# Optimization experiments

Hardware: AMD Instinct MI355X
Metric: run time of the kernel (lower is better)

## Reference

```python
import jax, jax.numpy as jnp
import numpy as np

NEG_SLOPE = 0.2

def setup_inputs() -> dict:
    key = jax.random.key(0)
    ks = jax.random.split(key, 10)
    N, E, L, D, H = 100000, 3200000, 200000, 128, 128
    x = jax.random.normal(ks[0], (N, D), dtype=jnp.float32)
    edge_index = jax.random.randint(ks[1], (2, E), 0, N, dtype=jnp.int64)
    edge_label_index = jax.random.randint(ks[2], (2, L), 0, N, dtype=jnp.int64)
    s = 1.0 / np.sqrt(D)
    W1l = jax.random.uniform(ks[3], (D, H), minval=-s, maxval=s, dtype=jnp.float32)
    b1 = jax.random.uniform(ks[4], (H,), minval=-s, maxval=s, dtype=jnp.float32)
    W1r = jax.random.uniform(ks[5], (D, H), minval=-s, maxval=s, dtype=jnp.float32)
    s2 = 1.0 / np.sqrt(H)
    W2l = jax.random.uniform(ks[6], (H, H), minval=-s2, maxval=s2, dtype=jnp.float32)
    b2 = jax.random.uniform(ks[7], (H,), minval=-s2, maxval=s2, dtype=jnp.float32)
    W2r = jax.random.uniform(ks[8], (H, H), minval=-s2, maxval=s2, dtype=jnp.float32)
    return {"x": x, "edge_index": edge_index, "edge_label_index": edge_label_index,
            "W1l": W1l, "b1": b1, "W1r": W1r, "W2l": W2l, "b2": b2, "W2r": W2r}

def reference(x, edge_index, edge_label_index, W1l, b1, W1r, W2l, b2, W2r):
    N = x.shape[0]
    src, dst = edge_index[0], edge_index[1]
    # in-degree for mean aggregation (clamped to avoid div-by-zero, matching mean over empty = 0)
    deg = jax.ops.segment_sum(jnp.ones_like(dst, dtype=x.dtype), dst, num_segments=N)
    inv_deg = (1.0 / jnp.maximum(deg, 1.0))[:, None]

    def sage(h, Wl, b, Wr):
        # mean of source-node features over incoming edges at each target node
        agg = jax.ops.segment_sum(h[src], dst, num_segments=N) * inv_deg
        return agg @ Wl + b + h @ Wr

    h = sage(x, W1l, b1, W1r)
    h = jnp.where(h >= 0, h, NEG_SLOPE * h)  # leaky_relu; eval mode so no dropout
    h = sage(h, W2l, b2, W2r)
    x_src = h[edge_label_index[0]]
    x_trg = h[edge_label_index[1]]
    return jnp.sum(x_src * x_trg, axis=1)
```

## Files before the change

kernel.cpp:

```cpp
#include <hip/hip_runtime.h>
#include <hip/hip_fp16.h>


#define D128 128
#define BSHIFT 9
#define BNODES 512

typedef __bf16 bf16x8 __attribute__((ext_vector_type(8)));
typedef float  f32x4  __attribute__((ext_vector_type(4)));
typedef _Float16 h2   __attribute__((ext_vector_type(2)));

union uh2cast { unsigned u; h2 h; };
__device__ inline h2 uash2(unsigned u) { uh2cast c; c.u = u; return c.h; }

__device__ inline unsigned short f2bf(float f) {
    unsigned u = __float_as_uint(f);
    u = u + 0x7FFF + ((u >> 16) & 1);
    return (unsigned short)(u >> 16);
}
__device__ inline float bf2f(unsigned short s) {
    return __uint_as_float(((unsigned)s) << 16);
}
__device__ inline unsigned packbf2(float lo, float hi) {
    return (unsigned)f2bf(lo) | ((unsigned)f2bf(hi) << 16);
}
__device__ inline unsigned char f2e5(float f) {
    unsigned short h = __half_as_ushort(__float2half(f));
    h = (unsigned short)(h + 0x7F + ((h >> 8) & 1));
    return (unsigned char)(h >> 8);
}


__global__ void cast_kernel(const float* __restrict__ in, unsigned short* __restrict__ outb,
                            unsigned char* __restrict__ out8, int n4) {
    int i = blockIdx.x * blockDim.x + threadIdx.x;
    if (i >= n4) return;
    float4 v = ((const float4*)in)[i];
    ushort4 ob;
    ob.x = f2bf(v.x); ob.y = f2bf(v.y); ob.z = f2bf(v.z); ob.w = f2bf(v.w);
    ((ushort4*)outb)[i] = ob;
    unsigned p = (unsigned)f2e5(v.x) | ((unsigned)f2e5(v.y) << 8) |
                 ((unsigned)f2e5(v.z) << 16) | ((unsigned)f2e5(v.w) << 24);
    ((unsigned*)out8)[i] = p;
}


__global__ void repack_kernel(const float* __restrict__ W1l, const float* __restrict__ W1r,
                              const float* __restrict__ W2l, const float* __restrict__ W2r,
                              unsigned short* __restrict__ packed) {
    int tid = blockIdx.x * blockDim.x + threadIdx.x;
    int layer = tid >> 15;
    int r = tid & 32767;
    int j    = r & 7;
    int lane = (r >> 3) & 63;
    int nt   = (r >> 9) & 7;
    int kc   = (r >> 12) & 7;
    int k   = kc * 32 + ((lane >> 4) << 3) + j;
    int col = nt * 16 + (lane & 15);
    const float* Wl = layer ? W2l : W1l;
    const float* Wr = layer ? W2r : W1r;
    float v = (k < 128) ? Wl[k * 128 + col] : Wr[(k - 128) * 128 + col];
    packed[tid] = f2bf(v);
}


__global__ void hist_kernel(const int* __restrict__ dst, int* __restrict__ gcnt,
                            int E, int NB) {
    __shared__ int h[256];
    int t = threadIdx.x;
    h[t] = 0;
    __syncthreads();
    int base = blockIdx.x * 8192;
#pragma unroll
    for (int k = 0; k < 32; ++k) {
        int e = base + k * 256 + t;
        if (e < E) atomicAdd(&h[dst[e] >> BSHIFT], 1);
    }
    __syncthreads();
    if (t < NB && h[t]) atomicAdd(&gcnt[t], h[t]);
}

__global__ void bucket_scan(const int* __restrict__ gcnt, int* __restrict__ bucket_base,
                            int* __restrict__ bucket_cur, int* __restrict__ rowptr,
                            int NB, int N, int E) {
    __shared__ int sc[256];
    __shared__ int orig[256];
    int t = threadIdx.x;
    int v = (t < NB) ? gcnt[t] : 0;
    orig[t] = v;
    sc[t] = v;
    __syncthreads();
    for (int off = 1; off < 256; off <<= 1) {
        int a = (t >= off) ? sc[t - off] : 0;
        __syncthreads();
        sc[t] += a;
        __syncthreads();
    }
    int ex = sc[t] - orig[t];
    if (t < NB) { bucket_base[t] = ex; bucket_cur[t] = ex; }
    if (t == 0) { bucket_base[NB] = E; rowptr[N] = E; }
}

__global__ void scatter_kernel(const int* __restrict__ src, const int* __restrict__ dst,
                               int* __restrict__ bucket_cur, int* __restrict__ pairs,
                               int E, int NB) {
    __shared__ int hist[256], lscan[256], gbase[256];
    __shared__ int lsrc[1024], ldst[1024];
    int t = threadIdx.x;
    hist[t] = 0;
    __syncthreads();
    int base = blockIdx.x * 1024;
    int total = E - base; if (total > 1024) total = 1024;

    int ms[4], md[4], mb[4], mr[4];
#pragma unroll
    for (int k = 0; k < 4; ++k) {
        int i = k * 256 + t;
        int e = base + i;
        mb[k] = -1;
        if (i < total) {
            ms[k] = src[e];
            md[k] = dst[e];
            mb[k] = md[k] >> BSHIFT;
            mr[k] = atomicAdd(&hist[mb[k]], 1);
        }
    }
    __syncthreads();
    lscan[t] = hist[t];
    __syncthreads();
    for (int off = 1; off < 256; off <<= 1) {
        int a = (t >= off) ? lscan[t - off] : 0;
        __syncthreads();
        lscan[t] += a;
        __syncthreads();
    }
    lscan[t] -= hist[t];
    if (t < NB && hist[t] > 0) gbase[t] = atomicAdd(&bucket_cur[t], hist[t]);
    __syncthreads();
#pragma unroll
    for (int k = 0; k < 4; ++k) {
        if (mb[k] >= 0) {
            int idx = lscan[mb[k]] + mr[k];
            lsrc[idx] = ms[k];
            ldst[idx] = md[k];
        }
    }
    __syncthreads();
#pragma unroll
    for (int k = 0; k < 4; ++k) {
        int i = k * 256 + t;
        if (i < total) {
            int d = ldst[i];
            int b = d >> BSHIFT;
            int pos = gbase[b] + (i - lscan[b]);
            pairs[pos] = (lsrc[i] << BSHIFT) | (d & (BNODES - 1));
        }
    }
}

__global__ void bucket_fill(const int* __restrict__ pairs, const int* __restrict__ bucket_base,
                            int* __restrict__ rowptr, int* __restrict__ srcs, int N) {
    __shared__ int hist[BNODES], excl[BNODES], sc[BNODES];
    int b = blockIdx.x;
    int t = threadIdx.x;
    int node0 = b << BSHIFT;
    int pbeg = bucket_base[b];
    int pend = bucket_base[b + 1];
    hist[t] = 0;
    __syncthreads();
    for (int p = pbeg + t; p < pend; p += BNODES) {
        atomicAdd(&hist[pairs[p] & (BNODES - 1)], 1);
    }
    __syncthreads();
    sc[t] = hist[t];
    __syncthreads();
    for (int off = 1; off < BNODES; off <<= 1) {
        int a = (t >= off) ? sc[t - off] : 0;
        __syncthreads();
        sc[t] += a;
        __syncthreads();
    }
    excl[t] = sc[t] - hist[t];
    int node = node0 + t;
    if (node < N) rowptr[node] = pbeg + excl[t];
    __syncthreads();
    hist[t] = 0;
    __syncthreads();
    for (int p = pbeg + t; p < pend; p += BNODES) {
        int w = pairs[p];
        int dl = w & (BNODES - 1);
        int c = atomicAdd(&hist[dl], 1);
        srcs[pbeg + excl[dl] + c] = ((unsigned)w) >> BSHIFT;
    }
}


__device__ inline void pkacc8(h2* A, uint2 v) {
    A[0] += uash2((v.x << 8) & 0xFF00FF00u);
    A[1] += uash2(v.x & 0xFF00FF00u);
    A[2] += uash2((v.y << 8) & 0xFF00FF00u);
    A[3] += uash2(v.y & 0xFF00FF00u);
}

__global__ void agg_kernel(const int* __restrict__ rowptr, const int* __restrict__ srcs,
                           const unsigned char* __restrict__ feat8,
                           unsigned short* __restrict__ out, int N) {
    int wave = threadIdx.x >> 6;
    int lane = threadIdx.x & 63;
    int q  = lane >> 4;
    int ql = lane & 15;
    int n = blockIdx.x * 4 + wave;
    if (n >= N) return;
    int beg = rowptr[n];
    int end = rowptr[n + 1];
    const uint2* f = (const uint2*)feat8;

    h2 A0[4], A1[4], A2[4], A3[4];
    h2 z; z[0] = (_Float16)0.f; z[1] = (_Float16)0.f;
#pragma unroll
    for (int k = 0; k < 4; ++k) { A0[k] = z; A1[k] = z; A2[k] = z; A3[k] = z; }

    int j = beg;
    for (; j + 16 <= end; j += 16) {
        int e0 = srcs[j + q];
        int e1 = srcs[j + 4 + q];
        int e2 = srcs[j + 8 + q];
        int e3 = srcs[j + 12 + q];
        uint2 v0 = f[(size_t)e0 * 16 + ql];
        uint2 v1 = f[(size_t)e1 * 16 + ql];
        uint2 v2 = f[(size_t)e2 * 16 + ql];
        uint2 v3 = f[(size_t)e3 * 16 + ql];
        pkacc8(A0, v0);
        pkacc8(A1, v1);
        pkacc8(A2, v2);
        pkacc8(A3, v3);
    }
    for (; j + 4 <= end; j += 4) {
        int e = srcs[j + q];
        uint2 v = f[(size_t)e * 16 + ql];
        pkacc8(A0, v);
    }
    int rem = end - j;
    if (q < rem) {
        int e = srcs[j + q];
        uint2 v = f[(size_t)e * 16 + ql];
        pkacc8(A1, v);
    }

    float c[8];
#pragma unroll
    for (int p = 0; p < 4; ++p) {
        float lo = (float)A0[p][0] + (float)A1[p][0] + (float)A2[p][0] + (float)A3[p][0];
        float hi = (float)A0[p][1] + (float)A1[p][1] + (float)A2[p][1] + (float)A3[p][1];
        int base = (p >> 1) * 4 + (p & 1);
        c[base] = lo;
        c[base + 2] = hi;
    }

#pragma unroll
    for (int k = 0; k < 8; ++k) {
        c[k] += __shfl_xor(c[k], 16, 64);
        c[k] += __shfl_xor(c[k], 32, 64);
    }

    int deg = end - beg;
    float inv = deg > 0 ? 1.0f / (float)deg : 0.f;
    if (q == 0) {
        uint4 r;
        r.x = packbf2(c[0] * inv, c[1] * inv);
        r.y = packbf2(c[2] * inv, c[3] * inv);
        r.z = packbf2(c[4] * inv, c[5] * inv);
        r.w = packbf2(c[6] * inv, c[7] * inv);
        ((uint4*)out)[(size_t)n * 16 + ql] = r;
    }
}


template <bool LEAKY>
__global__ void mm_kernel(const unsigned short* __restrict__ A,
                          const unsigned short* __restrict__ F,
                          const unsigned short* __restrict__ Wp,
                          const float* __restrict__ bias,
                          unsigned short* __restrict__ out,
                          unsigned char* __restrict__ out8, int N) {
    int wid = threadIdx.x >> 6;
    int lane = threadIdx.x & 63;
    int quad = lane >> 4;
    int m0 = (blockIdx.x * 4 + wid) * 32;

    int rowA0 = m0 + (lane & 15);
    int rowA1 = rowA0 + 16;
    if (rowA0 > N - 1) rowA0 = N - 1;
    if (rowA1 > N - 1) rowA1 = N - 1;

    f32x4 acc[2][8];
#pragma unroll
    for (int t = 0; t < 2; ++t)
#pragma unroll
        for (int nt = 0; nt < 8; ++nt) acc[t][nt] = (f32x4){0.f, 0.f, 0.f, 0.f};

#pragma unroll
    for (int kc = 0; kc < 8; ++kc) {
        const unsigned short* src = (kc < 4) ? (A + kc * 32) : (F + (kc - 4) * 32);
        bf16x8 af0 = *(const bf16x8*)(src + (size_t)rowA0 * D128 + quad * 8);
        bf16x8 af1 = *(const bf16x8*)(src + (size_t)rowA1 * D128 + quad * 8);
        const unsigned short* wp = Wp + ((size_t)kc * 8) * 512 + lane * 8;
#pragma unroll
        for (int nt = 0; nt < 8; ++nt) {
            bf16x8 bf = *(const bf16x8*)(wp + nt * 512);
            acc[0][nt] = __builtin_amdgcn_mfma_f32_16x16x32_bf16(af0, bf, acc[0][nt], 0, 0, 0);
            acc[1][nt] = __builtin_amdgcn_mfma_f32_16x16x32_bf16(af1, bf, acc[1][nt], 0, 0, 0);
        }
    }

#pragma unroll
    for (int nt = 0; nt < 8; ++nt) {
        int col = nt * 16 + (lane & 15);
        float bv = bias[col];
#pragma unroll
        for (int t = 0; t < 2; ++t) {
#pragma unroll
            for (int r = 0; r < 4; ++r) {
                int row = m0 + t * 16 + quad * 4 + r;
                if (row < N) {
                    float v = acc[t][nt][r] + bv;
                    if (LEAKY) v = v >= 0.f ? v : 0.2f * v;
                    out[(size_t)row * D128 + col] = f2bf(v);
                    if (out8) out8[(size_t)row * D128 + col] = f2e5(v);
                }
            }
        }
    }
}


__global__ void score_kernel(const int* __restrict__ eli, const unsigned short* __restrict__ h,
                             float* __restrict__ out, int L) {
    int wave = threadIdx.x >> 6;
    int lane = threadIdx.x & 63;
    int l0 = (blockIdx.x * 4 + wave) * 4;
    if (l0 >= L) return;
    const ushort2* h2p = (const ushort2*)h;
    int a[4], b[4];
#pragma unroll
    for (int k = 0; k < 4; ++k) {
        int l = l0 + k;
        if (l > L - 1) l = L - 1;
        a[k] = eli[l];
        b[k] = eli[L + l];
    }
    float p[4];
#pragma unroll
    for (int k = 0; k < 4; ++k) {
        ushort2 u = h2p[(size_t)a[k] * 64 + lane];
        ushort2 v = h2p[(size_t)b[k] * 64 + lane];
        p[k] = bf2f(u.x) * bf2f(v.x) + bf2f(u.y) * bf2f(v.y);
    }
#pragma unroll
    for (int off = 32; off > 0; off >>= 1) {
#pragma unroll
        for (int k = 0; k < 4; ++k) p[k] += __shfl_down(p[k], off, 64);
    }
    if (lane == 0) {
#pragma unroll
        for (int k = 0; k < 4; ++k) {
            if (l0 + k < L) out[l0 + k] = p[k];
        }
    }
}


extern "C" void kernel_launch(void* const* d_in, const int* in_sizes, int n_in,
                              void* d_out, int out_size, void* d_ws, size_t ws_size,
                              hipStream_t stream) {
    const float* x   = (const float*)d_in[0];
    const int*   ei  = (const int*)d_in[1];
    const int*   eli = (const int*)d_in[2];
    const float* W1l = (const float*)d_in[3];
    const float* b1  = (const float*)d_in[4];
    const float* W1r = (const float*)d_in[5];
    const float* W2l = (const float*)d_in[6];
    const float* b2  = (const float*)d_in[7];
    const float* W2r = (const float*)d_in[8];

    const int N = in_sizes[0] / D128;
    const int E = in_sizes[1] / 2;
    const int L = in_sizes[2] / 2;
    const int* srcp = ei;
    const int* dstp = ei + E;
    const int NB = (N + BNODES - 1) >> BSHIFT;

    char* ws = (char*)d_ws;
    size_t off = 0;
    auto alloc = [&](size_t bytes) -> void* {
        void* p = ws + off;
        off += (bytes + 255) & ~(size_t)255;
        return p;
    };
    int*   rowptr = (int*)alloc((size_t)(N + 1) * sizeof(int));
    int*   gcnt   = (int*)alloc(256 * sizeof(int));
    int*   bbase  = (int*)alloc(257 * sizeof(int));
    int*   bcur   = (int*)alloc(256 * sizeof(int));
    int*   pairs  = (int*)alloc((size_t)E * sizeof(int));
    int*   srcs   = (int*)alloc((size_t)E * sizeof(int));
    unsigned short* xb   = (unsigned short*)alloc((size_t)N * D128 * 2);
    unsigned char*  x8   = (unsigned char*)alloc((size_t)N * D128);
    unsigned char*  h1f8 = (unsigned char*)alloc((size_t)N * D128);
    unsigned short* aggb = (unsigned short*)alloc((size_t)N * D128 * 2);
    unsigned short* h1b  = (unsigned short*)alloc((size_t)N * D128 * 2);
    unsigned short* h2b  = (unsigned short*)alloc((size_t)N * D128 * 2);
    unsigned short* Wp   = (unsigned short*)alloc(2 * 32768 * 2);
    (void)ws_size; (void)n_in; (void)out_size;

    int n4 = N * D128 / 4;
    cast_kernel<<<(n4 + 255) / 256, 256, 0, stream>>>(x, xb, x8, n4);
    repack_kernel<<<65536 / 256, 256, 0, stream>>>(W1l, W1r, W2l, W2r, Wp);

    hipMemsetAsync(gcnt, 0, 256 * sizeof(int), stream);
    hist_kernel<<<(E + 8191) / 8192, 256, 0, stream>>>(dstp, gcnt, E, NB);
    bucket_scan<<<1, 256, 0, stream>>>(gcnt, bbase, bcur, rowptr, NB, N, E);
    scatter_kernel<<<(E + 1023) / 1024, 256, 0, stream>>>(srcp, dstp, bcur, pairs, E, NB);
    bucket_fill<<<NB, BNODES, 0, stream>>>(pairs, bbase, rowptr, srcs, N);

    agg_kernel<<<(N + 3) / 4, 256, 0, stream>>>(rowptr, srcs, x8, aggb, N);
    mm_kernel<true><<<(N + 127) / 128, 256, 0, stream>>>(aggb, xb, Wp, b1, h1b, h1f8, N);

    agg_kernel<<<(N + 3) / 4, 256, 0, stream>>>(rowptr, srcs, h1f8, aggb, N);
    mm_kernel<false><<<(N + 127) / 128, 256, 0, stream>>>(aggb, h1b, Wp + 32768, b2, h2b,
                                                          (unsigned char*)nullptr, N);

    score_kernel<<<(L + 15) / 16, 256, 0, stream>>>(eli, h2b, (float*)d_out, L);
}
```

Measured before the change: 454.4 us.

## Fuse prep kernels, drop global histogram atomics, vectorize aggregation index loads

Merges the cast, weight repack and histogram kernels into a single launch. Each histogram block now writes its own partial counts, which the scan kernel sums, so the memset and global atomics go away. The aggregation kernel reads source indices as int4 after an alignment prologue, and the indices are stored pre-multiplied by 16 to avoid per-load index multiplication. In exchange, the single-block scan loops serially over about 391 partial rows, and the int indices limit node count times 16 to the int range.

```diff
diff --git a/kernel.cpp b/kernel.cpp
--- a/kernel.cpp
+++ b/kernel.cpp
@@ -31,62 +31,66 @@
 }
 
 
-__global__ void cast_kernel(const float* __restrict__ in, unsigned short* __restrict__ outb,
-                            unsigned char* __restrict__ out8, int n4) {
-    int i = blockIdx.x * blockDim.x + threadIdx.x;
-    if (i >= n4) return;
-    float4 v = ((const float4*)in)[i];
-    ushort4 ob;
-    ob.x = f2bf(v.x); ob.y = f2bf(v.y); ob.z = f2bf(v.z); ob.w = f2bf(v.w);
-    ((ushort4*)outb)[i] = ob;
-    unsigned p = (unsigned)f2e5(v.x) | ((unsigned)f2e5(v.y) << 8) |
-                 ((unsigned)f2e5(v.z) << 16) | ((unsigned)f2e5(v.w) << 24);
-    ((unsigned*)out8)[i] = p;
-}
-
-
-__global__ void repack_kernel(const float* __restrict__ W1l, const float* __restrict__ W1r,
-                              const float* __restrict__ W2l, const float* __restrict__ W2r,
-                              unsigned short* __restrict__ packed) {
-    int tid = blockIdx.x * blockDim.x + threadIdx.x;
-    int layer = tid >> 15;
-    int r = tid & 32767;
-    int j    = r & 7;
-    int lane = (r >> 3) & 63;
-    int nt   = (r >> 9) & 7;
-    int kc   = (r >> 12) & 7;
-    int k   = kc * 32 + ((lane >> 4) << 3) + j;
-    int col = nt * 16 + (lane & 15);
-    const float* Wl = layer ? W2l : W1l;
-    const float* Wr = layer ? W2r : W1r;
-    float v = (k < 128) ? Wl[k * 128 + col] : Wr[(k - 128) * 128 + col];
-    packed[tid] = f2bf(v);
-}
-
-
-__global__ void hist_kernel(const int* __restrict__ dst, int* __restrict__ gcnt,
-                            int E, int NB) {
-    __shared__ int h[256];
+__global__ void prep_kernel(const float* __restrict__ in, unsigned short* __restrict__ outb,
+                            unsigned char* __restrict__ out8, int n4,
+                            const float* __restrict__ W1l, const float* __restrict__ W1r,
+                            const float* __restrict__ W2l, const float* __restrict__ W2r,
+                            unsigned short* __restrict__ packed,
+                            const int* __restrict__ dst, int* __restrict__ bh,
+                            int E, int castBlocks, int histBlocks) {
+    int bid = blockIdx.x;
     int t = threadIdx.x;
-    h[t] = 0;
-    __syncthreads();
-    int base = blockIdx.x * 8192;
-#pragma unroll
-    for (int k = 0; k < 32; ++k) {
-        int e = base + k * 256 + t;
-        if (e < E) atomicAdd(&h[dst[e] >> BSHIFT], 1);
-    }
-    __syncthreads();
-    if (t < NB && h[t]) atomicAdd(&gcnt[t], h[t]);
-}
-
-__global__ void bucket_scan(const int* __restrict__ gcnt, int* __restrict__ bucket_base,
-                            int* __restrict__ bucket_cur, int* __restrict__ rowptr,
-                            int NB, int N, int E) {
+    if (bid < castBlocks) {
+        int i = bid * 256 + t;
+        if (i >= n4) return;
+        float4 v = ((const float4*)in)[i];
+        ushort4 ob;
+        ob.x = f2bf(v.x); ob.y = f2bf(v.y); ob.z = f2bf(v.z); ob.w = f2bf(v.w);
+        ((ushort4*)outb)[i] = ob;
+        unsigned p = (unsigned)f2e5(v.x) | ((unsigned)f2e5(v.y) << 8) |
+                     ((unsigned)f2e5(v.z) << 16) | ((unsigned)f2e5(v.w) << 24);
+        ((unsigned*)out8)[i] = p;
+    } else if (bid < castBlocks + 256) {
+        int tid = (bid - castBlocks) * 256 + t;
+        int layer = tid >> 15;
+        int r = tid & 32767;
+        int j    = r & 7;
+        int lane = (r >> 3) & 63;
+        int nt   = (r >> 9) & 7;
+        int kc   = (r >> 12) & 7;
+        int k   = kc * 32 + ((lane >> 4) << 3) + j;
+        int col = nt * 16 + (lane & 15);
+        const float* Wl = layer ? W2l : W1l;
+        const float* Wr = layer ? W2r : W1r;
+        float v = (k < 128) ? Wl[k * 128 + col] : Wr[(k - 128) * 128 + col];
+        packed[tid] = f2bf(v);
+    } else {
+        __shared__ int h[256];
+        int hb = bid - castBlocks - 256;
+        if (hb >= histBlocks) return;
+        h[t] = 0;
+        __syncthreads();
+        int base = hb * 8192;
+#pragma unroll
+        for (int k = 0; k < 32; ++k) {
+            int e = base + k * 256 + t;
+            if (e < E) atomicAdd(&h[dst[e] >> BSHIFT], 1);
+        }
+        __syncthreads();
+        bh[hb * 256 + t] = h[t];
+    }
+}
+
+
+__global__ void bucket_scan(const int* __restrict__ bh, int nhb,
+                            int* __restrict__ bucket_base, int* __restrict__ bucket_cur,
+                            int* __restrict__ rowptr, int NB, int N, int E) {
     __shared__ int sc[256];
     __shared__ int orig[256];
     int t = threadIdx.x;
-    int v = (t < NB) ? gcnt[t] : 0;
+    int v = 0;
+    for (int b = 0; b < nhb; ++b) v += bh[b * 256 + t];
+    if (t >= NB) v = 0;
     orig[t] = v;
     sc[t] = v;
     __syncthreads();
@@ -190,7 +194,7 @@
         int w = pairs[p];
         int dl = w & (BNODES - 1);
         int c = atomicAdd(&hist[dl], 1);
-        srcs[pbeg + excl[dl] + c] = ((unsigned)w) >> BSHIFT;
+        srcs[pbeg + excl[dl] + c] = (int)(((unsigned)w) >> BSHIFT) << 4;
     }
 }
 
@@ -221,30 +225,33 @@
     for (int k = 0; k < 4; ++k) { A0[k] = z; A1[k] = z; A2[k] = z; A3[k] = z; }
 
     int j = beg;
+    int pre = (4 - (beg & 3)) & 3;
+    if (pre > end - beg) pre = end - beg;
+    if (q < pre) {
+        uint2 v = f[srcs[j + q] + ql];
+        pkacc8(A1, v);
+    }
+    j += pre;
+
     for (; j + 16 <= end; j += 16) {
-        int e0 = srcs[j + q];
-        int e1 = srcs[j + 4 + q];
-        int e2 = srcs[j + 8 + q];
-        int e3 = srcs[j + 12 + q];
-        uint2 v0 = f[(size_t)e0 * 16 + ql];
-        uint2 v1 = f[(size_t)e1 * 16 + ql];
-        uint2 v2 = f[(size_t)e2 * 16 + ql];
-        uint2 v3 = f[(size_t)e3 * 16 + ql];
+        int4 e = *(const int4*)(srcs + j + 4 * q);
+        uint2 v0 = f[e.x + ql];
+        uint2 v1 = f[e.y + ql];
+        uint2 v2 = f[e.z + ql];
+        uint2 v3 = f[e.w + ql];
         pkacc8(A0, v0);
         pkacc8(A1, v1);
         pkacc8(A2, v2);
         pkacc8(A3, v3);
     }
     for (; j + 4 <= end; j += 4) {
-        int e = srcs[j + q];
-        uint2 v = f[(size_t)e * 16 + ql];
+        uint2 v = f[srcs[j + q] + ql];
         pkacc8(A0, v);
     }
     int rem = end - j;
     if (q < rem) {
-        int e = srcs[j + q];
-        uint2 v = f[(size_t)e * 16 + ql];
-        pkacc8(A1, v);
+        uint2 v = f[srcs[j + q] + ql];
+        pkacc8(A2, v);
     }
 
     float c[8];
@@ -397,12 +404,13 @@
         off += (bytes + 255) & ~(size_t)255;
         return p;
     };
+    const int histBlocks = (E + 8191) / 8192;
     int*   rowptr = (int*)alloc((size_t)(N + 1) * sizeof(int));
-    int*   gcnt   = (int*)alloc(256 * sizeof(int));
+    int*   bh     = (int*)alloc((size_t)histBlocks * 256 * sizeof(int));
     int*   bbase  = (int*)alloc(257 * sizeof(int));
     int*   bcur   = (int*)alloc(256 * sizeof(int));
     int*   pairs  = (int*)alloc((size_t)E * sizeof(int));
-    int*   srcs   = (int*)alloc((size_t)E * sizeof(int));
+    int*   srcs   = (int*)alloc(((size_t)E + 16) * sizeof(int));
     unsigned short* xb   = (unsigned short*)alloc((size_t)N * D128 * 2);
     unsigned char*  x8   = (unsigned char*)alloc((size_t)N * D128);
     unsigned char*  h1f8 = (unsigned char*)alloc((size_t)N * D128);
@@ -413,12 +421,11 @@
     (void)ws_size; (void)n_in; (void)out_size;
 
     int n4 = N * D128 / 4;
-    cast_kernel<<<(n4 + 255) / 256, 256, 0, stream>>>(x, xb, x8, n4);
-    repack_kernel<<<65536 / 256, 256, 0, stream>>>(W1l, W1r, W2l, W2r, Wp);
-
-    hipMemsetAsync(gcnt, 0, 256 * sizeof(int), stream);
-    hist_kernel<<<(E + 8191) / 8192, 256, 0, stream>>>(dstp, gcnt, E, NB);
-    bucket_scan<<<1, 256, 0, stream>>>(gcnt, bbase, bcur, rowptr, NB, N, E);
+    int castBlocks = (n4 + 255) / 256;
+    prep_kernel<<<castBlocks + 256 + histBlocks, 256, 0, stream>>>(
+        x, xb, x8, n4, W1l, W1r, W2l, W2r, Wp, dstp, bh, E, castBlocks, histBlocks);
+
+    bucket_scan<<<1, 256, 0, stream>>>(bh, histBlocks, bbase, bcur, rowptr, NB, N, E);
     scatter_kernel<<<(E + 1023) / 1024, 256, 0, stream>>>(srcp, dstp, bcur, pairs, E, NB);
     bucket_fill<<<NB, BNODES, 0, stream>>>(pairs, bbase, rowptr, srcs, N);
 
```

Measured after the change: 510.9 us. 1.12x slower.
